# Kernel tuning notes

Measured on AMD Instinct MI355X. Metric: run time of the kernel, lower is better.

The kernel has to match this reference:

```python
import jax, jax.numpy as jnp
import numpy as np

EPS = 1e-5

def layer_norm(x, gamma, beta):
    mu = jnp.mean(x, axis=-1, keepdims=True)
    var = jnp.mean(jnp.square(x - mu), axis=-1, keepdims=True)
    return (x - mu) * jax.lax.rsqrt(var + EPS) * gamma + beta

def setup_inputs() -> dict:
    key = jax.random.key(0)
    ks = jax.random.split(key, 12)
    B, N, F, H, K = 32, 2048, 128, 256, 64
    A_hat = jax.random.uniform(ks[0], (B, N, N), dtype=jnp.float32) / N  # row-normalized-ish adjacency
    X = jax.random.normal(ks[1], (B, N, F), dtype=jnp.float32)
    def lin(k, din, dout):
        s = 1.0 / np.sqrt(din)
        k1, k2 = jax.random.split(k)
        W = jax.random.uniform(k1, (din, dout), minval=-s, maxval=s, dtype=jnp.float32)
        b = jax.random.uniform(k2, (dout,), minval=-s, maxval=s, dtype=jnp.float32)
        return W, b
    W1, b1 = lin(ks[2], F, H)
    W2, b2 = lin(ks[3], H, H)
    Wa, ba = lin(ks[4], H, K)
    Wl, bl = lin(ks[5], H, K)
    g1 = jnp.ones((H,), jnp.float32); beta1 = jnp.zeros((H,), jnp.float32)
    g2 = jnp.ones((H,), jnp.float32); beta2 = jnp.zeros((H,), jnp.float32)
    return {"A_hat": A_hat, "X": X, "W1": W1, "b1": b1, "g1": g1, "beta1": beta1,
            "W2": W2, "b2": b2, "g2": g2, "beta2": beta2,
            "Wa": Wa, "ba": ba, "Wl": Wl, "bl": bl}

def reference(A_hat, X, W1, b1, g1, beta1, W2, b2, g2, beta2, Wa, ba, Wl, bl):
    # Layer 1: aggregate -> linear -> LayerNorm -> ReLU (dropout is eval identity)
    H = jnp.einsum('bnm,bmf->bnf', A_hat, X)
    H = jnp.einsum('bnf,fh->bnh', H, W1) + b1
    H = jax.nn.relu(layer_norm(H, g1, beta1))
    # Layer 2
    H = jnp.einsum('bnm,bmh->bnh', A_hat, H)
    H = jnp.einsum('bnh,hk->bnk', H, W2) + b2
    H = jax.nn.relu(layer_norm(H, g2, beta2))
    # mean readout over nodes
    g = jnp.mean(H, axis=1)
    pred_arr_reg = g @ Wa + ba
    logits = g @ Wl + bl
    return (pred_arr_reg, logits)
```

## Files before the change

kernel.cpp:

```cpp
#include <hip/hip_runtime.h>
#include <hip/hip_bf16.h>

#define NN 2048

typedef __attribute__((ext_vector_type(4))) float f32x4;
typedef __attribute__((ext_vector_type(8))) short bf16x8;

__device__ __forceinline__ unsigned short f2bf(float f) {
  __hip_bfloat16 h = __float2bfloat16(f);
  return __builtin_bit_cast(unsigned short, h);
}
__device__ __forceinline__ unsigned int pk2(float a, float b) {
  return (unsigned int)f2bf(a) | ((unsigned int)f2bf(b) << 16);
}
__device__ __forceinline__ void gld_lds16(const void* g, void* l) {
  __builtin_amdgcn_global_load_lds(
      (const __attribute__((address_space(1))) unsigned int*)g,
      (__attribute__((address_space(3))) unsigned int*)l, 16, 0, 0);
}

__global__ void k_tr_all(const float* __restrict__ X, unsigned short* __restrict__ XT,
                         const float* __restrict__ W1, unsigned short* __restrict__ W1T,
                         const float* __restrict__ W2, unsigned short* __restrict__ W2T) {
  int bid = blockIdx.x;
  const float* src;
  unsigned short* dst;
  int R, C, bx, by, b;
  if (bid < 8192) {
    src = X; dst = XT; R = 2048; C = 128;
    b = bid >> 8;
    int r = bid & 255;
    bx = r & 63; by = r >> 6;
  } else if (bid < 8192 + 32) {
    src = W1; dst = W1T; R = 128; C = 256; b = 0;
    int r = bid - 8192;
    bx = r & 3; by = r >> 2;
  } else {
    src = W2; dst = W2T; R = 256; C = 256; b = 0;
    int r = bid - 8224;
    bx = r & 7; by = r >> 3;
  }
  src += (size_t)b * R * C;
  dst += (size_t)b * R * C;
  __shared__ float tile[32][33];
  int r0 = bx * 32, c0 = by * 32;
  int t = threadIdx.x;
  int r = t >> 3, c4 = (t & 7) << 2;
  float4 v = *(const float4*)(src + (size_t)(r0 + r) * C + c0 + c4);
  tile[r][c4 + 0] = v.x; tile[r][c4 + 1] = v.y; tile[r][c4 + 2] = v.z; tile[r][c4 + 3] = v.w;
  __syncthreads();
  ushort4 o;
  o.x = f2bf(tile[c4 + 0][r]); o.y = f2bf(tile[c4 + 1][r]);
  o.z = f2bf(tile[c4 + 2][r]); o.w = f2bf(tile[c4 + 3][r]);
  *(ushort4*)(dst + (size_t)(c0 + r) * R + r0 + c4) = o;
}

#define AGG_STEP(KT, AREGC, AREGN, CUR, VMC)                                   \
  {                                                                            \
    const int kt_ = (KT);                                                      \
    if (kt_ < NKT - 1) {    \
      _Pragma("unroll") for (int i = 0; i < NF; ++i) {                         \
        int jj = i * 512 + t;                                                  \
        int n_ = jj >> 3, s_ = jj & 7, sp_ = s_ ^ (n_ & 7);                    \
        gld_lds16(BTb + (size_t)n_ * NN + (size_t)(kt_ + 1) * 64 + sp_ * 8,    \
                  &Bs[(CUR) ^ 1][(i * 512 + wid * 64) * 8]);                   \
      }                                                                        \
    }                                                                          \
    __builtin_amdgcn_sched_barrier(0);      \
    if (kt_ < NKT - 2) {    \
      const float* p_ = apb + (size_t)(kt_ + 2) * 64;                          \
      _Pragma("unroll") for (int j = 0; j < 4; ++j)                            \
          AREGN[j] = ((const float4*)p_)[j];                                   \
    }                                                                          \
    if (kt_ < NKT - 1) {    \
      _Pragma("unroll") for (int i = 0; i < 2; ++i) {                          \
        uint4 w_;                                                              \
        w_.x = pk2(AREGC[2 * i].x, AREGC[2 * i].y);                            \
        w_.y = pk2(AREGC[2 * i].z, AREGC[2 * i].w);                            \
        w_.z = pk2(AREGC[2 * i + 1].x, AREGC[2 * i + 1].y);                    \
        w_.w = pk2(AREGC[2 * i + 1].z, AREGC[2 * i + 1].w);                    \
        int s_ = ak * 2 + i, sp_ = s_ ^ (ar & 7);                              \
        *(uint4*)&As[(CUR) ^ 1][(ar * 8 + sp_) * 8] = w_;                      \
      }                                                                        \
    }                                                                          \
    _Pragma("unroll") for (int kh = 0; kh < 2; ++kh) {                         \
      bf16x8 af[4], bfr[NF];                                                   \
      _Pragma("unroll") for (int mi = 0; mi < 4; ++mi) {                       \
        int row = wr * 64 + mi * 16 + lr;                                      \
        int sp_ = (kh * 4 + q) ^ (row & 7);                                    \
        af[mi] = *(const bf16x8*)&As[CUR][(row * 8 + sp_) * 8];                \
      }                                                                        \
      _Pragma("unroll") for (int ni = 0; ni < NF; ++ni) {                      \
        int brow = wc * WN + ni * 16 + lr;                                     \
        int sp_ = (kh * 4 + q) ^ (brow & 7);                                   \
        bfr[ni] = *(const bf16x8*)&Bs[CUR][(brow * 8 + sp_) * 8];              \
      }                                                                        \
      _Pragma("unroll") for (int mi = 0; mi < 4; ++mi)                         \
        _Pragma("unroll") for (int ni = 0; ni < NF; ++ni)                      \
          acc[mi][ni] = __builtin_amdgcn_mfma_f32_16x16x32_bf16(               \
              af[mi], bfr[ni], acc[mi][ni], 0, 0, 0);                          \
    }                                                                          \
    asm volatile("s_waitcnt vmcnt(" #VMC ") lgkmcnt(0)" ::: "memory");         \
    __builtin_amdgcn_s_barrier();                                              \
  }

template <int NCOLS, int MODE>
__global__ __launch_bounds__(512, NCOLS == 128 ? 4 : 2) void k_agg_fused(
    const float* __restrict__ A, const unsigned short* __restrict__ BT,
    const unsigned short* __restrict__ WT, const float* __restrict__ bias,
    const float* __restrict__ gamma, const float* __restrict__ beta,
    unsigned short* __restrict__ HTout, float* __restrict__ gpart) {
  constexpr int WN = NCOLS / 4;
  constexpr int NF = NCOLS / 64;
  constexpr int NKT = NN / 64;
  constexpr int FIN = NCOLS;
  constexpr int NQT = FIN / 64;
  constexpr int NMB = NN / 128;

  __shared__ __align__(16) unsigned short As[2][128 * 64];
  __shared__ __align__(16) unsigned short Bs[2][NCOLS * 64];
  __shared__ float red[2][128][4];

  int L = blockIdx.x + gridDim.x * blockIdx.z;
  int xcd = L & 7, slot = L >> 3;
  int mb = slot % NMB;
  int b = xcd + 8 * (slot / NMB);
  int m0 = mb * 128;

  const float* Ab = A + (size_t)b * NN * NN;
  const unsigned short* BTb = BT + (size_t)b * (size_t)NCOLS * NN;
  int t = threadIdx.x, lane = t & 63, wid = t >> 6;
  int wr = wid >> 2, wc = wid & 3;
  int q = lane >> 4, lr = lane & 15;
  int ar = t >> 2, ak = t & 3;
  const float* apb = Ab + (size_t)(m0 + ar) * NN + ak * 16;

  f32x4 acc[4][NF] = {};
  float4 aregA[4], aregB[4];

  {
#pragma unroll
    for (int j = 0; j < 4; ++j) aregA[j] = ((const float4*)apb)[j];
#pragma unroll
    for (int i = 0; i < NF; ++i) {
      int jj = i * 512 + t;
      int n = jj >> 3, s = jj & 7, sp = s ^ (n & 7);
      gld_lds16(BTb + (size_t)n * NN + sp * 8, &Bs[0][(i * 512 + wid * 64) * 8]);
    }
#pragma unroll
    for (int i = 0; i < 2; ++i) {
      uint4 w;
      w.x = pk2(aregA[2 * i].x, aregA[2 * i].y);
      w.y = pk2(aregA[2 * i].z, aregA[2 * i].w);
      w.z = pk2(aregA[2 * i + 1].x, aregA[2 * i + 1].y);
      w.w = pk2(aregA[2 * i + 1].z, aregA[2 * i + 1].w);
      int s = ak * 2 + i, sp = s ^ (ar & 7);
      *(uint4*)&As[0][(ar * 8 + sp) * 8] = w;
    }
    __builtin_amdgcn_sched_barrier(0);
#pragma unroll
    for (int j = 0; j < 4; ++j) aregB[j] = ((const float4*)(apb + 64))[j];
    asm volatile("s_waitcnt vmcnt(4) lgkmcnt(0)" ::: "memory");
    __builtin_amdgcn_s_barrier();
  }

  for (int k2 = 0; k2 < NKT / 2 - 1; ++k2) {
    AGG_STEP(2 * k2, aregB, aregA, 0, 4);
    AGG_STEP(2 * k2 + 1, aregA, aregB, 1, 4);
  }
  AGG_STEP(NKT - 2, aregB, aregA, 0, 0);
  AGG_STEP(NKT - 1, aregA, aregB, 1, 0);

  unsigned short* Hs = (NCOLS == 128) ? &As[0][0] : &Bs[0][0];
  unsigned short* Ws = (NCOLS == 128) ? &Bs[0][0] : &As[0][0];
#pragma unroll
  for (int mi = 0; mi < 4; ++mi) {
#pragma unroll
    for (int ni = 0; ni < NF; ++ni) {
#pragma unroll
      for (int j = 0; j < 4; ++j) {
        int row = wr * 64 + mi * 16 + q * 4 + j;
        int col = wc * WN + ni * 16 + lr;
        int sp = (col >> 3) ^ (row & 7);
        Hs[row * FIN + sp * 8 + (col & 7)] = f2bf(acc[mi][ni][j]);
      }
    }
  }

  f32x4 acc2[4][4] = {};
  for (int qt = 0; qt < NQT; ++qt) {
    __syncthreads();
#pragma unroll
    for (int i = 0; i < 4; ++i) {
      int jj = i * 512 + t;
      int h = jj >> 3, s = jj & 7, sp = s ^ (h & 7);
      gld_lds16(WT + (size_t)h * FIN + qt * 64 + sp * 8, Ws + (i * 512 + wid * 64) * 8);
    }
    __syncthreads();
#pragma unroll
    for (int kh = 0; kh < 2; ++kh) {
      bf16x8 hf[4], wf[4];
#pragma unroll
      for (int mi = 0; mi < 4; ++mi) {
        int row = wr * 64 + mi * 16 + lr;
        int slotk = qt * 8 + kh * 4 + q;
        int sp = slotk ^ (row & 7);
        hf[mi] = *(const bf16x8*)&Hs[row * FIN + sp * 8];
      }
#pragma unroll
      for (int ni = 0; ni < 4; ++ni) {
        int h = wc * 64 + ni * 16 + lr;
        int sp = (kh * 4 + q) ^ (h & 7);
        wf[ni] = *(const bf16x8*)&Ws[(h * 8 + sp) * 8];
      }
#pragma unroll
      for (int mi = 0; mi < 4; ++mi) {
#pragma unroll
        for (int ni = 0; ni < 4; ++ni)
          acc2[mi][ni] = __builtin_amdgcn_mfma_f32_16x16x32_bf16(hf[mi], wf[ni], acc2[mi][ni], 0, 0, 0);
      }
    }
  }

  float bcol[4], gcol[4], zcol[4];
#pragma unroll
  for (int ni = 0; ni < 4; ++ni) {
    int col = wc * 64 + ni * 16 + lr;
    bcol[ni] = bias[col]; gcol[ni] = gamma[col]; zcol[ni] = beta[col];
  }
#pragma unroll
  for (int mi = 0; mi < 4; ++mi) {
#pragma unroll
    for (int j = 0; j < 4; ++j) {
      float s = 0.f, ss = 0.f;
#pragma unroll
      for (int ni = 0; ni < 4; ++ni) {
        float v = acc2[mi][ni][j] + bcol[ni];
        acc2[mi][ni][j] = v;
        s += v; ss += v * v;
      }
#pragma unroll
      for (int m = 1; m < 16; m <<= 1) { s += __shfl_xor(s, m); ss += __shfl_xor(ss, m); }
      if (lr == 0) {
        int rl = wr * 64 + mi * 16 + q * 4 + j;
        red[0][rl][wc] = s;
        red[1][rl][wc] = ss;
      }
    }
  }
  __syncthreads();
#pragma unroll
  for (int mi = 0; mi < 4; ++mi) {
#pragma unroll
    for (int j = 0; j < 4; ++j) {
      int rl = wr * 64 + mi * 16 + q * 4 + j;
      float s = red[0][rl][0] + red[0][rl][1] + red[0][rl][2] + red[0][rl][3];
      float ss = red[1][rl][0] + red[1][rl][1] + red[1][rl][2] + red[1][rl][3];
      float mean = s * (1.f / 256.f);
      float var = ss * (1.f / 256.f) - mean * mean;
      float inv = rsqrtf(var + 1e-5f);
#pragma unroll
      for (int ni = 0; ni < 4; ++ni) {
        float v = (acc2[mi][ni][j] - mean) * inv * gcol[ni] + zcol[ni];
        acc2[mi][ni][j] = v > 0.f ? v : 0.f;
      }
    }
  }
  if (MODE == 0) {
#pragma unroll
    for (int mi = 0; mi < 4; ++mi) {
#pragma unroll
      for (int ni = 0; ni < 4; ++ni) {
        int col = wc * 64 + ni * 16 + lr;
        int rowb = m0 + wr * 64 + mi * 16 + q * 4;
        ushort4 o;
        o.x = f2bf(acc2[mi][ni][0]); o.y = f2bf(acc2[mi][ni][1]);
        o.z = f2bf(acc2[mi][ni][2]); o.w = f2bf(acc2[mi][ni][3]);
        *(ushort4*)(HTout + ((size_t)b * 256 + col) * NN + rowb) = o;
      }
    }
  } else {
#pragma unroll
    for (int ni = 0; ni < 4; ++ni) {
      float cs = 0.f;
#pragma unroll
      for (int mi = 0; mi < 4; ++mi) {
#pragma unroll
        for (int j = 0; j < 4; ++j) cs += acc2[mi][ni][j];
      }
      cs += __shfl_xor(cs, 16);
      cs += __shfl_xor(cs, 32);
      if (q == 0) {
        int col = wc * 64 + ni * 16 + lr;
        gpart[(((size_t)b * NMB + mb) * 2 + wr) * 256 + col] = cs;
      }
    }
  }
}

__global__ __launch_bounds__(512, 4) void k_agg2(
    const float* __restrict__ A, const unsigned short* __restrict__ BT,
    const unsigned short* __restrict__ WT, const float* __restrict__ bias,
    const float* __restrict__ gamma, const float* __restrict__ beta,
    float* __restrict__ gpart) {
  constexpr int NKT = 32;
  constexpr int NMB = 16;

  __shared__ __align__(16) unsigned short As1[128 * 64];
  __shared__ __align__(16) unsigned short Bs[2][256 * 64];
  float* redp = (float*)As1;

  int L = blockIdx.x + gridDim.x * blockIdx.z;
  int xcd = L & 7, slot = L >> 3;
  int mb = slot % NMB;
  int b = xcd + 8 * (slot / NMB);
  int m0 = mb * 128;

  const float* Ab = A + (size_t)b * NN * NN;
  const unsigned short* BTb = BT + (size_t)b * (size_t)256 * NN;
  int t = threadIdx.x, lane = t & 63, wid = t >> 6;
  int wr = wid >> 2, wc = wid & 3;
  int q = lane >> 4, lr = lane & 15;
  int ar = t >> 2, ak = t & 3;
  const float* apb = Ab + (size_t)(m0 + ar) * NN + ak * 16;

  f32x4 acc[4][4] = {};
  float4 areg[4];

  {
#pragma unroll
    for (int j = 0; j < 4; ++j) areg[j] = ((const float4*)apb)[j];
#pragma unroll
    for (int i = 0; i < 4; ++i) {
      int jj = i * 512 + t;
      int n = jj >> 3, s = jj & 7, sp = s ^ (n & 7);
      gld_lds16(BTb + (size_t)n * NN + sp * 8, &Bs[0][(i * 512 + wid * 64) * 8]);
    }
#pragma unroll
    for (int i = 0; i < 2; ++i) {
      uint4 w;
      w.x = pk2(areg[2 * i].x, areg[2 * i].y);
      w.y = pk2(areg[2 * i].z, areg[2 * i].w);
      w.z = pk2(areg[2 * i + 1].x, areg[2 * i + 1].y);
      w.w = pk2(areg[2 * i + 1].z, areg[2 * i + 1].w);
      int s = ak * 2 + i, sp = s ^ (ar & 7);
      *(uint4*)&As1[(ar * 8 + sp) * 8] = w;
    }
    asm volatile("s_waitcnt vmcnt(0) lgkmcnt(0)" ::: "memory");
    __builtin_amdgcn_s_barrier();
  }

  for (int kt = 0; kt < NKT; ++kt) {
    int cur = kt & 1;
    unsigned short* bnx = &Bs[cur ^ 1][0];
    const unsigned short* bcu = &Bs[cur][0];
    if (kt < NKT - 1) {
#pragma unroll
      for (int i = 0; i < 4; ++i) {
        int jj = i * 512 + t;
        int n = jj >> 3, s = jj & 7, sp = s ^ (n & 7);
        gld_lds16(BTb + (size_t)n * NN + (size_t)(kt + 1) * 64 + sp * 8,
                  bnx + (i * 512 + wid * 64) * 8);
      }
    }
    __builtin_amdgcn_sched_barrier(0);
    if (kt < NKT - 1) {
      const float* p = apb + (size_t)(kt + 1) * 64;
#pragma unroll
      for (int j = 0; j < 4; ++j) areg[j] = ((const float4*)p)[j];
    }
#pragma unroll
    for (int kh = 0; kh < 2; ++kh) {
      bf16x8 af[4], bfr[4];
#pragma unroll
      for (int mi = 0; mi < 4; ++mi) {
        int row = wr * 64 + mi * 16 + lr;
        int sp = (kh * 4 + q) ^ (row & 7);
        af[mi] = *(const bf16x8*)&As1[(row * 8 + sp) * 8];
      }
#pragma unroll
      for (int ni = 0; ni < 4; ++ni) {
        int brow = wc * 64 + ni * 16 + lr;
        int sp = (kh * 4 + q) ^ (brow & 7);
        bfr[ni] = *(const bf16x8*)(bcu + (brow * 8 + sp) * 8);
      }
#pragma unroll
      for (int mi = 0; mi < 4; ++mi)
#pragma unroll
        for (int ni = 0; ni < 4; ++ni)
          acc[mi][ni] = __builtin_amdgcn_mfma_f32_16x16x32_bf16(af[mi], bfr[ni], acc[mi][ni], 0, 0, 0);
    }
    asm volatile("s_waitcnt lgkmcnt(0)" ::: "memory");
    __builtin_amdgcn_s_barrier();
    __builtin_amdgcn_sched_barrier(0);
    if (kt < NKT - 1) {
#pragma unroll
      for (int i = 0; i < 2; ++i) {
        uint4 w;
        w.x = pk2(areg[2 * i].x, areg[2 * i].y);
        w.y = pk2(areg[2 * i].z, areg[2 * i].w);
        w.z = pk2(areg[2 * i + 1].x, areg[2 * i + 1].y);
        w.w = pk2(areg[2 * i + 1].z, areg[2 * i + 1].w);
        int s = ak * 2 + i, sp = s ^ (ar & 7);
        *(uint4*)&As1[(ar * 8 + sp) * 8] = w;
      }
    }
    asm volatile("s_waitcnt vmcnt(0) lgkmcnt(0)" ::: "memory");
    __builtin_amdgcn_s_barrier();
  }

  unsigned short* Hs = &Bs[0][0];
#pragma unroll
  for (int mi = 0; mi < 4; ++mi) {
#pragma unroll
    for (int ni = 0; ni < 4; ++ni) {
#pragma unroll
      for (int j = 0; j < 4; ++j) {
        int row = wr * 64 + mi * 16 + q * 4 + j;
        int col = wc * 64 + ni * 16 + lr;
        int sp = (col >> 3) ^ (row & 7);
        Hs[row * 256 + sp * 8 + (col & 7)] = f2bf(acc[mi][ni][j]);
      }
    }
  }

  f32x4 acc2[4][4] = {};
  for (int qt = 0; qt < 8; ++qt) {
    asm volatile("s_waitcnt lgkmcnt(0)" ::: "memory");
    __builtin_amdgcn_s_barrier();
#pragma unroll
    for (int i = 0; i < 2; ++i) {
      int jj = i * 512 + t;
      int h = jj >> 2, spp = jj & 3, spl = spp ^ (h & 3);
      gld_lds16(WT + (size_t)h * 256 + qt * 32 + spl * 8,
                &As1[(i * 512 + wid * 64) * 8]);
    }
    asm volatile("s_waitcnt vmcnt(0) lgkmcnt(0)" ::: "memory");
    __builtin_amdgcn_s_barrier();
    bf16x8 hf[4], wf[4];
#pragma unroll
    for (int mi = 0; mi < 4; ++mi) {
      int row = wr * 64 + mi * 16 + lr;
      int slotk = qt * 4 + q;
      int sp = slotk ^ (row & 7);
      hf[mi] = *(const bf16x8*)&Hs[row * 256 + sp * 8];
    }
#pragma unroll
    for (int ni = 0; ni < 4; ++ni) {
      int h = wc * 64 + ni * 16 + lr;
      int sp = q ^ (h & 3);
      wf[ni] = *(const bf16x8*)&As1[(h * 4 + sp) * 8];
    }
#pragma unroll
    for (int mi = 0; mi < 4; ++mi)
#pragma unroll
      for (int ni = 0; ni < 4; ++ni)
        acc2[mi][ni] = __builtin_amdgcn_mfma_f32_16x16x32_bf16(hf[mi], wf[ni], acc2[mi][ni], 0, 0, 0);
  }
  asm volatile("s_waitcnt lgkmcnt(0)" ::: "memory");
  __builtin_amdgcn_s_barrier();

  float bcol[4], gcol[4], zcol[4];
#pragma unroll
  for (int ni = 0; ni < 4; ++ni) {
    int col = wc * 64 + ni * 16 + lr;
    bcol[ni] = bias[col]; gcol[ni] = gamma[col]; zcol[ni] = beta[col];
  }
#pragma unroll
  for (int mi = 0; mi < 4; ++mi) {
#pragma unroll
    for (int j = 0; j < 4; ++j) {
      float s = 0.f, ss = 0.f;
#pragma unroll
      for (int ni = 0; ni < 4; ++ni) {
        float v = acc2[mi][ni][j] + bcol[ni];
        acc2[mi][ni][j] = v;
        s += v; ss += v * v;
      }
#pragma unroll
      for (int m = 1; m < 16; m <<= 1) { s += __shfl_xor(s, m); ss += __shfl_xor(ss, m); }
      if (lr == 0) {
        int rl = wr * 64 + mi * 16 + q * 4 + j;
        redp[(0 * 128 + rl) * 4 + wc] = s;
        redp[(1 * 128 + rl) * 4 + wc] = ss;
      }
    }
  }
  __syncthreads();
#pragma unroll
  for (int mi = 0; mi < 4; ++mi) {
#pragma unroll
    for (int j = 0; j < 4; ++j) {
      int rl = wr * 64 + mi * 16 + q * 4 + j;
      float s = redp[(0 * 128 + rl) * 4 + 0] + redp[(0 * 128 + rl) * 4 + 1] +
                redp[(0 * 128 + rl) * 4 + 2] + redp[(0 * 128 + rl) * 4 + 3];
      float ss = redp[(1 * 128 + rl) * 4 + 0] + redp[(1 * 128 + rl) * 4 + 1] +
                 redp[(1 * 128 + rl) * 4 + 2] + redp[(1 * 128 + rl) * 4 + 3];
      float mean = s * (1.f / 256.f);
      float var = ss * (1.f / 256.f) - mean * mean;
      float inv = rsqrtf(var + 1e-5f);
#pragma unroll
      for (int ni = 0; ni < 4; ++ni) {
        float v = (acc2[mi][ni][j] - mean) * inv * gcol[ni] + zcol[ni];
        acc2[mi][ni][j] = v > 0.f ? v : 0.f;
      }
    }
  }
#pragma unroll
  for (int ni = 0; ni < 4; ++ni) {
    float cs = 0.f;
#pragma unroll
    for (int mi = 0; mi < 4; ++mi) {
#pragma unroll
      for (int j = 0; j < 4; ++j) cs += acc2[mi][ni][j];
    }
    cs += __shfl_xor(cs, 16);
    cs += __shfl_xor(cs, 32);
    if (q == 0) {
      int col = wc * 64 + ni * 16 + lr;
      gpart[(((size_t)b * NMB + mb) * 2 + wr) * 256 + col] = cs;
    }
  }
}

__global__ void k_readout(const float* __restrict__ gpart, const float* __restrict__ Wa,
                          const float* __restrict__ ba, const float* __restrict__ Wl,
                          const float* __restrict__ bl, float* __restrict__ out) {
  __shared__ float gl[256];
  int b = blockIdx.x, t = threadIdx.x;
  float s = 0.f;
#pragma unroll 4
  for (int p = 0; p < 32; ++p) s += gpart[((size_t)b * 32 + p) * 256 + t];
  gl[t] = s * (1.f / 2048.f);
  __syncthreads();
  if (t < 128) {
    int k = t & 63;
    const float* W = (t >= 64) ? Wl : Wa;
    const float* bb = (t >= 64) ? bl : ba;
    float a = 0.f;
    for (int h = 0; h < 256; ++h) a += gl[h] * W[h * 64 + k];
    a += bb[k];
    out[((t >= 64) ? 2048 : 0) + b * 64 + k] = a;
  }
}

extern "C" void kernel_launch(void* const* d_in, const int* in_sizes, int n_in,
                              void* d_out, int out_size, void* d_ws, size_t ws_size,
                              hipStream_t stream) {
  const float* A_hat = (const float*)d_in[0];
  const float* X   = (const float*)d_in[1];
  const float* W1  = (const float*)d_in[2];
  const float* b1  = (const float*)d_in[3];
  const float* g1  = (const float*)d_in[4];
  const float* be1 = (const float*)d_in[5];
  const float* W2  = (const float*)d_in[6];
  const float* b2  = (const float*)d_in[7];
  const float* g2  = (const float*)d_in[8];
  const float* be2 = (const float*)d_in[9];
  const float* Wa  = (const float*)d_in[10];
  const float* ba  = (const float*)d_in[11];
  const float* Wl  = (const float*)d_in[12];
  const float* bl  = (const float*)d_in[13];

  char* ws = (char*)d_ws;
  const size_t MB = 1024 * 1024;
  unsigned short* XT  = (unsigned short*)(ws);
  unsigned short* H1T = (unsigned short*)(ws + 16 * MB);
  unsigned short* W1T = (unsigned short*)(ws + 48 * MB);
  unsigned short* W2T = (unsigned short*)(ws + 48 * MB + 256 * 1024);
  float* gpart        = (float*)(ws + 49 * MB);

  k_tr_all<<<dim3(8288), 256, 0, stream>>>(X, XT, W1, W1T, W2, W2T);
  k_agg_fused<128, 0><<<dim3(16, 1, 32), 512, 0, stream>>>(
      A_hat, XT, W1T, b1, g1, be1, H1T, nullptr);
  k_agg2<<<dim3(16, 1, 32), 512, 0, stream>>>(
      A_hat, H1T, W2T, b2, g2, be2, gpart);
  k_readout<<<dim3(32), 256, 0, stream>>>(gpart, Wa, ba, Wl, bl, (float*)d_out);
}
```

Measured before the change: 330.9 us.

## Triple-buffer B tiles and double-buffer A in agg2 with one barrier per step

```diff
diff --git a/kernel.cpp b/kernel.cpp
--- a/kernel.cpp
+++ b/kernel.cpp
@@ -298,17 +298,67 @@
   }
 }
 
-__global__ __launch_bounds__(512, 4) void k_agg2(
+#define AGG2_STEP(KT, AREGC, AREGN, BR, BS_, VMC)                              \
+  {                                                                            \
+    const int kt_ = (KT);                                                      \
+    if (kt_ < 30) {     \
+      _Pragma("unroll") for (int i = 0; i < 4; ++i) {                          \
+        int jj = i * 512 + t;                                                  \
+        int n_ = jj >> 3, s_ = jj & 7, sp_ = s_ ^ (n_ & 7);                    \
+        gld_lds16(BTb + (size_t)n_ * NN + (size_t)(kt_ + 2) * 64 + sp_ * 8,    \
+                  (BS_) + (i * 512 + wid * 64) * 8);                           \
+      }                                                                        \
+    }                                                                          \
+    __builtin_amdgcn_sched_barrier(0);      \
+    if (kt_ < 30) {                                      \
+      const float* p_ = apb + (size_t)(kt_ + 2) * 64;                          \
+      _Pragma("unroll") for (int j = 0; j < 4; ++j)                            \
+          AREGN[j] = ((const float4*)p_)[j];                                   \
+    }                                                                          \
+    if (kt_ < 31) {                           \
+      _Pragma("unroll") for (int i = 0; i < 2; ++i) {                          \
+        uint4 w_;                                                              \
+        w_.x = pk2(AREGC[2 * i].x, AREGC[2 * i].y);                            \
+        w_.y = pk2(AREGC[2 * i].z, AREGC[2 * i].w);                            \
+        w_.z = pk2(AREGC[2 * i + 1].x, AREGC[2 * i + 1].y);                    \
+        w_.w = pk2(AREGC[2 * i + 1].z, AREGC[2 * i + 1].w);                    \
+        int s_ = ak * 2 + i, sp_ = s_ ^ (ar & 7);                              \
+        *(uint4*)&As[(kt_ + 1) & 1][(ar * 8 + sp_) * 8] = w_;                  \
+      }                                                                        \
+    }                                                                          \
+    _Pragma("unroll") for (int kh = 0; kh < 2; ++kh) {                         \
+      bf16x8 af[4], bfr[4];                                                    \
+      _Pragma("unroll") for (int mi = 0; mi < 4; ++mi) {                       \
+        int row = wr * 64 + mi * 16 + lr;                                      \
+        int sp_ = (kh * 4 + q) ^ (row & 7);                                    \
+        af[mi] = *(const bf16x8*)&As[(KT) & 1][(row * 8 + sp_) * 8];           \
+      }                                                                        \
+      _Pragma("unroll") for (int ni = 0; ni < 4; ++ni) {                       \
+        int brow = wc * 64 + ni * 16 + lr;                                     \
+        int sp_ = (kh * 4 + q) ^ (brow & 7);                                   \
+        bfr[ni] = *(const bf16x8*)((BR) + (brow * 8 + sp_) * 8);               \
+      }                                                                        \
+      _Pragma("unroll") for (int mi = 0; mi < 4; ++mi)                         \
+        _Pragma("unroll") for (int ni = 0; ni < 4; ++ni)                       \
+          acc[mi][ni] = __builtin_amdgcn_mfma_f32_16x16x32_bf16(               \
+              af[mi], bfr[ni], acc[mi][ni], 0, 0, 0);                          \
+    }                                                                          \
+    asm volatile("s_waitcnt vmcnt(" #VMC ") lgkmcnt(0)" ::: "memory");         \
+    __builtin_amdgcn_s_barrier();                                              \
+  }
+
+#define ROT3() { unsigned short* tmp_ = bR; bR = bM; bM = bS; bS = tmp_; }
+
+__global__ __launch_bounds__(512, 2) void k_agg2(
     const float* __restrict__ A, const unsigned short* __restrict__ BT,
     const unsigned short* __restrict__ WT, const float* __restrict__ bias,
     const float* __restrict__ gamma, const float* __restrict__ beta,
     float* __restrict__ gpart) {
-  constexpr int NKT = 32;
   constexpr int NMB = 16;
 
-  __shared__ __align__(16) unsigned short As1[128 * 64];
-  __shared__ __align__(16) unsigned short Bs[2][256 * 64];
-  float* redp = (float*)As1;
+  __shared__ __align__(16) unsigned short As[2][128 * 64];
+  __shared__ __align__(16) unsigned short Bsb[3][256 * 64];
+  __shared__ float red[2][128][4];
 
   int L = blockIdx.x + gridDim.x * blockIdx.z;
   int xcd = L & 7, slot = L >> 3;
@@ -325,91 +375,55 @@
   const float* apb = Ab + (size_t)(m0 + ar) * NN + ak * 16;
 
   f32x4 acc[4][4] = {};
-  float4 areg[4];
+  float4 aregA[4], aregB[4];
+  unsigned short* bR = &Bsb[0][0];
+  unsigned short* bM = &Bsb[1][0];
+  unsigned short* bS = &Bsb[2][0];
 
   {
 #pragma unroll
-    for (int j = 0; j < 4; ++j) areg[j] = ((const float4*)apb)[j];
+    for (int j = 0; j < 4; ++j) aregA[j] = ((const float4*)apb)[j];
 #pragma unroll
     for (int i = 0; i < 4; ++i) {
       int jj = i * 512 + t;
       int n = jj >> 3, s = jj & 7, sp = s ^ (n & 7);
-      gld_lds16(BTb + (size_t)n * NN + sp * 8, &Bs[0][(i * 512 + wid * 64) * 8]);
+      gld_lds16(BTb + (size_t)n * NN + sp * 8, bR + (i * 512 + wid * 64) * 8);
     }
 #pragma unroll
     for (int i = 0; i < 2; ++i) {
       uint4 w;
-      w.x = pk2(areg[2 * i].x, areg[2 * i].y);
-      w.y = pk2(areg[2 * i].z, areg[2 * i].w);
-      w.z = pk2(areg[2 * i + 1].x, areg[2 * i + 1].y);
-      w.w = pk2(areg[2 * i + 1].z, areg[2 * i + 1].w);
+      w.x = pk2(aregA[2 * i].x, aregA[2 * i].y);
+      w.y = pk2(aregA[2 * i].z, aregA[2 * i].w);
+      w.z = pk2(aregA[2 * i + 1].x, aregA[2 * i + 1].y);
+      w.w = pk2(aregA[2 * i + 1].z, aregA[2 * i + 1].w);
       int s = ak * 2 + i, sp = s ^ (ar & 7);
-      *(uint4*)&As1[(ar * 8 + sp) * 8] = w;
-    }
-    asm volatile("s_waitcnt vmcnt(0) lgkmcnt(0)" ::: "memory");
+      *(uint4*)&As[0][(ar * 8 + sp) * 8] = w;
+    }
+    __builtin_amdgcn_sched_barrier(0);
+#pragma unroll
+    for (int j = 0; j < 4; ++j) aregB[j] = ((const float4*)(apb + 64))[j];
+#pragma unroll
+    for (int i = 0; i < 4; ++i) {
+      int jj = i * 512 + t;
+      int n = jj >> 3, s = jj & 7, sp = s ^ (n & 7);
+      gld_lds16(BTb + (size_t)n * NN + 64 + sp * 8, bM + (i * 512 + wid * 64) * 8);
+    }
+    asm volatile("s_waitcnt vmcnt(8) lgkmcnt(0)" ::: "memory");
     __builtin_amdgcn_s_barrier();
   }
 
-  for (int kt = 0; kt < NKT; ++kt) {
-    int cur = kt & 1;
-    unsigned short* bnx = &Bs[cur ^ 1][0];
-    const unsigned short* bcu = &Bs[cur][0];
-    if (kt < NKT - 1) {
-#pragma unroll
-      for (int i = 0; i < 4; ++i) {
-        int jj = i * 512 + t;
-        int n = jj >> 3, s = jj & 7, sp = s ^ (n & 7);
-        gld_lds16(BTb + (size_t)n * NN + (size_t)(kt + 1) * 64 + sp * 8,
-                  bnx + (i * 512 + wid * 64) * 8);
-      }
-    }
-    __builtin_amdgcn_sched_barrier(0);
-    if (kt < NKT - 1) {
-      const float* p = apb + (size_t)(kt + 1) * 64;
-#pragma unroll
-      for (int j = 0; j < 4; ++j) areg[j] = ((const float4*)p)[j];
-    }
-#pragma unroll
-    for (int kh = 0; kh < 2; ++kh) {
-      bf16x8 af[4], bfr[4];
-#pragma unroll
-      for (int mi = 0; mi < 4; ++mi) {
-        int row = wr * 64 + mi * 16 + lr;
-        int sp = (kh * 4 + q) ^ (row & 7);
-        af[mi] = *(const bf16x8*)&As1[(row * 8 + sp) * 8];
-      }
-#pragma unroll
-      for (int ni = 0; ni < 4; ++ni) {
-        int brow = wc * 64 + ni * 16 + lr;
-        int sp = (kh * 4 + q) ^ (brow & 7);
-        bfr[ni] = *(const bf16x8*)(bcu + (brow * 8 + sp) * 8);
-      }
-#pragma unroll
-      for (int mi = 0; mi < 4; ++mi)
-#pragma unroll
-        for (int ni = 0; ni < 4; ++ni)
-          acc[mi][ni] = __builtin_amdgcn_mfma_f32_16x16x32_bf16(af[mi], bfr[ni], acc[mi][ni], 0, 0, 0);
-    }
-    asm volatile("s_waitcnt lgkmcnt(0)" ::: "memory");
-    __builtin_amdgcn_s_barrier();
-    __builtin_amdgcn_sched_barrier(0);
-    if (kt < NKT - 1) {
-#pragma unroll
-      for (int i = 0; i < 2; ++i) {
-        uint4 w;
-        w.x = pk2(areg[2 * i].x, areg[2 * i].y);
-        w.y = pk2(areg[2 * i].z, areg[2 * i].w);
-        w.z = pk2(areg[2 * i + 1].x, areg[2 * i + 1].y);
-        w.w = pk2(areg[2 * i + 1].z, areg[2 * i + 1].w);
-        int s = ak * 2 + i, sp = s ^ (ar & 7);
-        *(uint4*)&As1[(ar * 8 + sp) * 8] = w;
-      }
-    }
-    asm volatile("s_waitcnt vmcnt(0) lgkmcnt(0)" ::: "memory");
-    __builtin_amdgcn_s_barrier();
-  }
-
-  unsigned short* Hs = &Bs[0][0];
+  for (int k2 = 0; k2 < 15; ++k2) {
+    AGG2_STEP(2 * k2, aregB, aregA, bR, bS, 8);
+    ROT3();
+    AGG2_STEP(2 * k2 + 1, aregA, aregB, bR, bS, 8);
+    ROT3();
+  }
+  AGG2_STEP(30, aregB, aregA, bR, bS, 0);
+  ROT3();
+  AGG2_STEP(31, aregA, aregB, bR, bS, 0);
+
+  unsigned short* Hs = &Bsb[0][0];
+  unsigned short* Ws = &As[0][0];
 #pragma unroll
   for (int mi = 0; mi < 4; ++mi) {
 #pragma unroll
@@ -425,40 +439,39 @@
   }
 
   f32x4 acc2[4][4] = {};
-  for (int qt = 0; qt < 8; ++qt) {
-    asm volatile("s_waitcnt lgkmcnt(0)" ::: "memory");
-    __builtin_amdgcn_s_barrier();
-#pragma unroll
-    for (int i = 0; i < 2; ++i) {
+  for (int qt = 0; qt < 4; ++qt) {
+    __syncthreads();
+#pragma unroll
+    for (int i = 0; i < 4; ++i) {
       int jj = i * 512 + t;
-      int h = jj >> 2, spp = jj & 3, spl = spp ^ (h & 3);
-      gld_lds16(WT + (size_t)h * 256 + qt * 32 + spl * 8,
-                &As1[(i * 512 + wid * 64) * 8]);
-    }
-    asm volatile("s_waitcnt vmcnt(0) lgkmcnt(0)" ::: "memory");
-    __builtin_amdgcn_s_barrier();
-    bf16x8 hf[4], wf[4];
-#pragma unroll
-    for (int mi = 0; mi < 4; ++mi) {
-      int row = wr * 64 + mi * 16 + lr;
-      int slotk = qt * 4 + q;
-      int sp = slotk ^ (row & 7);
-      hf[mi] = *(const bf16x8*)&Hs[row * 256 + sp * 8];
-    }
-#pragma unroll
-    for (int ni = 0; ni < 4; ++ni) {
-      int h = wc * 64 + ni * 16 + lr;
-      int sp = q ^ (h & 3);
-      wf[ni] = *(const bf16x8*)&As1[(h * 4 + sp) * 8];
-    }
-#pragma unroll
-    for (int mi = 0; mi < 4; ++mi)
-#pragma unroll
-      for (int ni = 0; ni < 4; ++ni)
-        acc2[mi][ni] = __builtin_amdgcn_mfma_f32_16x16x32_bf16(hf[mi], wf[ni], acc2[mi][ni], 0, 0, 0);
-  }
-  asm volatile("s_waitcnt lgkmcnt(0)" ::: "memory");
-  __builtin_amdgcn_s_barrier();
+      int h = jj >> 3, s = jj & 7, sp = s ^ (h & 7);
+      gld_lds16(WT + (size_t)h * 256 + qt * 64 + sp * 8, Ws + (i * 512 + wid * 64) * 8);
+    }
+    __syncthreads();
+#pragma unroll
+    for (int kh = 0; kh < 2; ++kh) {
+      bf16x8 hf[4], wf[4];
+#pragma unroll
+      for (int mi = 0; mi < 4; ++mi) {
+        int row = wr * 64 + mi * 16 + lr;
+        int slotk = qt * 8 + kh * 4 + q;
+        int sp = slotk ^ (row & 7);
+        hf[mi] = *(const bf16x8*)&Hs[row * 256 + sp * 8];
+      }
+#pragma unroll
+      for (int ni = 0; ni < 4; ++ni) {
+        int h = wc * 64 + ni * 16 + lr;
+        int sp = (kh * 4 + q) ^ (h & 7);
+        wf[ni] = *(const bf16x8*)&Ws[(h * 8 + sp) * 8];
+      }
+#pragma unroll
+      for (int mi = 0; mi < 4; ++mi) {
+#pragma unroll
+        for (int ni = 0; ni < 4; ++ni)
+          acc2[mi][ni] = __builtin_amdgcn_mfma_f32_16x16x32_bf16(hf[mi], wf[ni], acc2[mi][ni], 0, 0, 0);
+      }
+    }
+  }
 
   float bcol[4], gcol[4], zcol[4];
 #pragma unroll
@@ -481,8 +494,8 @@
       for (int m = 1; m < 16; m <<= 1) { s += __shfl_xor(s, m); ss += __shfl_xor(ss, m); }
       if (lr == 0) {
         int rl = wr * 64 + mi * 16 + q * 4 + j;
-        redp[(0 * 128 + rl) * 4 + wc] = s;
-        redp[(1 * 128 + rl) * 4 + wc] = ss;
+        red[0][rl][wc] = s;
+        red[1][rl][wc] = ss;
       }
     }
   }
@@ -492,10 +505,8 @@
 #pragma unroll
     for (int j = 0; j < 4; ++j) {
       int rl = wr * 64 + mi * 16 + q * 4 + j;
-      float s = redp[(0 * 128 + rl) * 4 + 0] + redp[(0 * 128 + rl) * 4 + 1] +
-                redp[(0 * 128 + rl) * 4 + 2] + redp[(0 * 128 + rl) * 4 + 3];
-      float ss = redp[(1 * 128 + rl) * 4 + 0] + redp[(1 * 128 + rl) * 4 + 1] +
-                 redp[(1 * 128 + rl) * 4 + 2] + redp[(1 * 128 + rl) * 4 + 3];
+      float s = red[0][rl][0] + red[0][rl][1] + red[0][rl][2] + red[0][rl][3];
+      float ss = red[1][rl][0] + red[1][rl][1] + red[1][rl][2] + red[1][rl][3];
       float mean = s * (1.f / 256.f);
       float var = ss * (1.f / 256.f) - mean * mean;
       float inv = rsqrtf(var + 1e-5f);
```

After: 325.1 us. About the same (-1.7%).

## Load A fragments directly into registers in agg2, dropping LDS staging of A

Applied to the files above, without the earlier changes.

```diff
diff --git a/kernel.cpp b/kernel.cpp
--- a/kernel.cpp
+++ b/kernel.cpp
@@ -303,12 +303,12 @@
     const unsigned short* __restrict__ WT, const float* __restrict__ bias,
     const float* __restrict__ gamma, const float* __restrict__ beta,
     float* __restrict__ gpart) {
-  constexpr int NKT = 32;
   constexpr int NMB = 16;
 
-  __shared__ __align__(16) unsigned short As1[128 * 64];
   __shared__ __align__(16) unsigned short Bs[2][256 * 64];
-  float* redp = (float*)As1;
+  __shared__ __align__(16) char wsregion[16 * 1024];
+  unsigned short* Ws = (unsigned short*)wsregion;
+  float* redp = (float*)wsregion;
 
   int L = blockIdx.x + gridDim.x * blockIdx.z;
   int xcd = L & 7, slot = L >> 3;
@@ -319,42 +319,31 @@
   const float* Ab = A + (size_t)b * NN * NN;
   const unsigned short* BTb = BT + (size_t)b * (size_t)256 * NN;
   int t = threadIdx.x, lane = t & 63, wid = t >> 6;
-  int wr = wid >> 2, wc = wid & 3;
   int q = lane >> 4, lr = lane & 15;
-  int ar = t >> 2, ak = t & 3;
-  const float* apb = Ab + (size_t)(m0 + ar) * NN + ak * 16;
-
-  f32x4 acc[4][4] = {};
+  const float* apl = Ab + (size_t)(m0 + wid * 16 + lr) * NN + q * 8;
+
+  f32x4 acc[16] = {};
   float4 areg[4];
 
   {
-#pragma unroll
-    for (int j = 0; j < 4; ++j) areg[j] = ((const float4*)apb)[j];
+    areg[0] = *(const float4*)(apl);
+    areg[1] = *(const float4*)(apl + 4);
+    areg[2] = *(const float4*)(apl + 32);
+    areg[3] = *(const float4*)(apl + 36);
 #pragma unroll
     for (int i = 0; i < 4; ++i) {
       int jj = i * 512 + t;
       int n = jj >> 3, s = jj & 7, sp = s ^ (n & 7);
       gld_lds16(BTb + (size_t)n * NN + sp * 8, &Bs[0][(i * 512 + wid * 64) * 8]);
     }
-#pragma unroll
-    for (int i = 0; i < 2; ++i) {
-      uint4 w;
-      w.x = pk2(areg[2 * i].x, areg[2 * i].y);
-      w.y = pk2(areg[2 * i].z, areg[2 * i].w);
-      w.z = pk2(areg[2 * i + 1].x, areg[2 * i + 1].y);
-      w.w = pk2(areg[2 * i + 1].z, areg[2 * i + 1].w);
-      int s = ak * 2 + i, sp = s ^ (ar & 7);
-      *(uint4*)&As1[(ar * 8 + sp) * 8] = w;
-    }
     asm volatile("s_waitcnt vmcnt(0) lgkmcnt(0)" ::: "memory");
     __builtin_amdgcn_s_barrier();
   }
 
-  for (int kt = 0; kt < NKT; ++kt) {
-    int cur = kt & 1;
-    unsigned short* bnx = &Bs[cur ^ 1][0];
-    const unsigned short* bcu = &Bs[cur][0];
-    if (kt < NKT - 1) {
+  for (int kt = 0; kt < 32; ++kt) {
+    const unsigned short* bcu = &Bs[kt & 1][0];
+    unsigned short* bnx = &Bs[(kt & 1) ^ 1][0];
+    if (kt < 31) {
 #pragma unroll
       for (int i = 0; i < 4; ++i) {
         int jj = i * 512 + t;
@@ -364,66 +353,55 @@
       }
     }
     __builtin_amdgcn_sched_barrier(0);
-    if (kt < NKT - 1) {
-      const float* p = apb + (size_t)(kt + 1) * 64;
-#pragma unroll
-      for (int j = 0; j < 4; ++j) areg[j] = ((const float4*)p)[j];
+    bf16x8 af0, af1;
+    {
+      uint4 u0, u1;
+      u0.x = pk2(areg[0].x, areg[0].y); u0.y = pk2(areg[0].z, areg[0].w);
+      u0.z = pk2(areg[1].x, areg[1].y); u0.w = pk2(areg[1].z, areg[1].w);
+      u1.x = pk2(areg[2].x, areg[2].y); u1.y = pk2(areg[2].z, areg[2].w);
+      u1.z = pk2(areg[3].x, areg[3].y); u1.w = pk2(areg[3].z, areg[3].w);
+      af0 = __builtin_bit_cast(bf16x8, u0);
+      af1 = __builtin_bit_cast(bf16x8, u1);
+    }
+    if (kt < 31) {
+      const float* p = apl + (size_t)(kt + 1) * 64;
+      areg[0] = *(const float4*)(p);
+      areg[1] = *(const float4*)(p + 4);
+      areg[2] = *(const float4*)(p + 32);
+      areg[3] = *(const float4*)(p + 36);
     }
 #pragma unroll
     for (int kh = 0; kh < 2; ++kh) {
-      bf16x8 af[4], bfr[4];
-#pragma unroll
-      for (int mi = 0; mi < 4; ++mi) {
-        int row = wr * 64 + mi * 16 + lr;
-        int sp = (kh * 4 + q) ^ (row & 7);
-        af[mi] = *(const bf16x8*)&As1[(row * 8 + sp) * 8];
-      }
-#pragma unroll
-      for (int ni = 0; ni < 4; ++ni) {
-        int brow = wc * 64 + ni * 16 + lr;
+      bf16x8 afk = kh ? af1 : af0;
+#pragma unroll
+      for (int ni = 0; ni < 16; ++ni) {
+        int brow = ni * 16 + lr;
         int sp = (kh * 4 + q) ^ (brow & 7);
-        bfr[ni] = *(const bf16x8*)(bcu + (brow * 8 + sp) * 8);
-      }
-#pragma unroll
-      for (int mi = 0; mi < 4; ++mi)
-#pragma unroll
-        for (int ni = 0; ni < 4; ++ni)
-          acc[mi][ni] = __builtin_amdgcn_mfma_f32_16x16x32_bf16(af[mi], bfr[ni], acc[mi][ni], 0, 0, 0);
-    }
-    asm volatile("s_waitcnt lgkmcnt(0)" ::: "memory");
+        bf16x8 bfr = *(const bf16x8*)(bcu + (brow * 8 + sp) * 8);
+        acc[ni] = __builtin_amdgcn_mfma_f32_16x16x32_bf16(afk, bfr, acc[ni], 0, 0, 0);
+      }
+    }
+    if (kt < 31) {
+      asm volatile("s_waitcnt vmcnt(4) lgkmcnt(0)" ::: "memory");
+    } else {
+      asm volatile("s_waitcnt vmcnt(0) lgkmcnt(0)" ::: "memory");
+    }
     __builtin_amdgcn_s_barrier();
-    __builtin_amdgcn_sched_barrier(0);
-    if (kt < NKT - 1) {
-#pragma unroll
-      for (int i = 0; i < 2; ++i) {
-        uint4 w;
-        w.x = pk2(areg[2 * i].x, areg[2 * i].y);
-        w.y = pk2(areg[2 * i].z, areg[2 * i].w);
-        w.z = pk2(areg[2 * i + 1].x, areg[2 * i + 1].y);
-        w.w = pk2(areg[2 * i + 1].z, areg[2 * i + 1].w);
-        int s = ak * 2 + i, sp = s ^ (ar & 7);
-        *(uint4*)&As1[(ar * 8 + sp) * 8] = w;
-      }
-    }
-    asm volatile("s_waitcnt vmcnt(0) lgkmcnt(0)" ::: "memory");
-    __builtin_amdgcn_s_barrier();
   }
 
   unsigned short* Hs = &Bs[0][0];
 #pragma unroll
-  for (int mi = 0; mi < 4; ++mi) {
-#pragma unroll
-    for (int ni = 0; ni < 4; ++ni) {
-#pragma unroll
-      for (int j = 0; j < 4; ++j) {
-        int row = wr * 64 + mi * 16 + q * 4 + j;
-        int col = wc * 64 + ni * 16 + lr;
-        int sp = (col >> 3) ^ (row & 7);
-        Hs[row * 256 + sp * 8 + (col & 7)] = f2bf(acc[mi][ni][j]);
-      }
-    }
-  }
-
+  for (int ni = 0; ni < 16; ++ni) {
+#pragma unroll
+    for (int j = 0; j < 4; ++j) {
+      int row = wid * 16 + q * 4 + j;
+      int col = ni * 16 + lr;
+      int sp = (col >> 3) ^ (row & 7);
+      Hs[row * 256 + sp * 8 + (col & 7)] = f2bf(acc[ni][j]);
+    }
+  }
+
+  int wr = wid >> 2, wc = wid & 3;
   f32x4 acc2[4][4] = {};
   for (int qt = 0; qt < 8; ++qt) {
     asm volatile("s_waitcnt lgkmcnt(0)" ::: "memory");
@@ -433,7 +411,7 @@
       int jj = i * 512 + t;
       int h = jj >> 2, spp = jj & 3, spl = spp ^ (h & 3);
       gld_lds16(WT + (size_t)h * 256 + qt * 32 + spl * 8,
-                &As1[(i * 512 + wid * 64) * 8]);
+                Ws + (i * 512 + wid * 64) * 8);
     }
     asm volatile("s_waitcnt vmcnt(0) lgkmcnt(0)" ::: "memory");
     __builtin_amdgcn_s_barrier();
@@ -449,7 +427,7 @@
     for (int ni = 0; ni < 4; ++ni) {
       int h = wc * 64 + ni * 16 + lr;
       int sp = q ^ (h & 3);
-      wf[ni] = *(const bf16x8*)&As1[(h * 4 + sp) * 8];
+      wf[ni] = *(const bf16x8*)&Ws[(h * 4 + sp) * 8];
     }
 #pragma unroll
     for (int mi = 0; mi < 4; ++mi)
```

Result: no change. 325.2 us (-1.7%).
